# Kernel tuning notes

Measured on AMD Instinct MI355X. Metric: run time of the kernel, lower is better.

Reference implementation:

```python
import jax, jax.numpy as jnp
import numpy as np
from jax import lax

L, H = 16384, 1024
EPS = 1e-5


def _ln(x, w, b):
    m = jnp.mean(x, axis=-1, keepdims=True)
    v = jnp.var(x, axis=-1, keepdims=True)
    return (x - m) * lax.rsqrt(v + EPS) * w + b


def setup_inputs() -> dict:
    key = jax.random.key(0)
    ks = jax.random.split(key, 12)
    s = 0.02
    return {
        "x": jax.random.normal(ks[0], (L, H), dtype=jnp.float32),
        "ln1_w": jnp.ones((H,), jnp.float32),
        "ln1_b": jnp.zeros((H,), jnp.float32),
        "W_in": jax.random.normal(ks[1], (H, H), jnp.float32) * s,
        "b_in": jnp.zeros((H,), jnp.float32),
        "W_gate": jax.random.normal(ks[2], (H, H), jnp.float32) * s,
        "b_gate": jnp.zeros((H,), jnp.float32),
        "W_out": jax.random.normal(ks[3], (H, H), jnp.float32) * s,
        "b_out": jnp.zeros((H,), jnp.float32),
        "state_decay": jnp.zeros((H,), jnp.float32),
        "ln2_w": jnp.ones((H,), jnp.float32),
        "ln2_b": jnp.zeros((H,), jnp.float32),
        "W_ff1": jax.random.normal(ks[4], (H, 2 * H), jnp.float32) * s,
        "b_ff1": jnp.zeros((2 * H,), jnp.float32),
        "W_ff2": jax.random.normal(ks[5], (2 * H, H), jnp.float32) * s,
        "b_ff2": jnp.zeros((H,), jnp.float32),
    }


def reference(x, ln1_w, ln1_b, W_in, b_in, W_gate, b_gate, W_out, b_out,
              state_decay, ln2_w, ln2_b, W_ff1, b_ff1, W_ff2, b_ff2):
    hidden = _ln(x, ln1_w, ln1_b)                       # [L,H]
    u = hidden @ W_in + b_in                            # [L,H]
    gate = jax.nn.sigmoid(hidden @ W_gate + b_gate)     # [L,H]
    decay = jax.nn.sigmoid(state_decay)                 # [H]

    def step(s, u_t):
        s = decay * s + u_t
        return s, s

    z = jnp.zeros((x.shape[1],), x.dtype)
    _, states_f = lax.scan(step, z, u)                  # forward recurrence
    _, states_b = lax.scan(step, z, u, reverse=True)    # backward recurrence
    state_out = 0.5 * (states_f + states_b) * gate

    x = x + state_out @ W_out + b_out
    h = _ln(x, ln2_w, ln2_b)
    x = x + jax.nn.silu(h @ W_ff1 + b_ff1) @ W_ff2 + b_ff2
    return x
```

## Files before the change

kernel.cpp:

```cpp
#include <hip/hip_runtime.h>
#include <hip/hip_bf16.h>
#include <hip/hip_fp16.h>

#define L_SEQ 16384
#define HDIM  1024
#define CH    32
#define NC    (L_SEQ / CH)

typedef _Float16 f16;
typedef _Float16 f16x8 __attribute__((ext_vector_type(8)));
typedef _Float16 f16x4 __attribute__((ext_vector_type(4)));
typedef float    f32x4 __attribute__((ext_vector_type(4)));

#define AS1(p) (const __attribute__((address_space(1))) void*)(p)
#define AS3(p) (__attribute__((address_space(3))) void*)(p)

__global__ __launch_bounds__(256) void wcvt_t(const float* __restrict__ in,
                                              f16* __restrict__ out, int K, int N) {
  __shared__ float tile[32][33];
  int n0 = blockIdx.x * 32, k0 = blockIdx.y * 32;
  int tx = threadIdx.x, ty = threadIdx.y;
#pragma unroll
  for (int i = 0; i < 4; i++) {
    int k = k0 + ty + i * 8;
    tile[ty + i * 8][tx] = in[(size_t)k * N + n0 + tx];
  }
  __syncthreads();
#pragma unroll
  for (int i = 0; i < 4; i++) {
    int n = n0 + ty + i * 8;
    out[(size_t)n * K + k0 + tx] = (f16)tile[tx][ty + i * 8];
  }
}

__global__ __launch_bounds__(256) void ln_k(const float* __restrict__ x,
                                            const float* __restrict__ w,
                                            const float* __restrict__ b,
                                            f16* __restrict__ out,
                                            f16* __restrict__ xcopy) {
  int row = blockIdx.x;
  int t = threadIdx.x;
  const float4* xr = (const float4*)(x + (size_t)row * HDIM);
  float4 v = xr[t];
  float s  = v.x + v.y + v.z + v.w;
  float s2 = v.x * v.x + v.y * v.y + v.z * v.z + v.w * v.w;
#pragma unroll
  for (int off = 32; off > 0; off >>= 1) {
    s  += __shfl_down(s, off);
    s2 += __shfl_down(s2, off);
  }
  __shared__ float red[8];
  int wid = t >> 6, lane = t & 63;
  if (lane == 0) { red[wid] = s; red[4 + wid] = s2; }
  __syncthreads();
  if (t == 0) {
    red[0] = red[0] + red[1] + red[2] + red[3];
    red[4] = red[4] + red[5] + red[6] + red[7];
  }
  __syncthreads();
  float mean = red[0] * (1.0f / HDIM);
  float var  = red[4] * (1.0f / HDIM) - mean * mean;
  float rstd = rsqrtf(var + 1e-5f);
  float4 ww = ((const float4*)w)[t];
  float4 bb = ((const float4*)b)[t];
  f16x4 o;
  o[0] = (f16)((v.x - mean) * rstd * ww.x + bb.x);
  o[1] = (f16)((v.y - mean) * rstd * ww.y + bb.y);
  o[2] = (f16)((v.z - mean) * rstd * ww.z + bb.z);
  o[3] = (f16)((v.w - mean) * rstd * ww.w + bb.w);
  ((f16x4*)(out + (size_t)row * HDIM))[t] = o;
  if (xcopy) {
    f16x4 c;
    c[0] = (f16)v.x; c[1] = (f16)v.y; c[2] = (f16)v.z; c[3] = (f16)v.w;
    ((f16x4*)(xcopy + (size_t)row * HDIM))[t] = c;
  }
}

__global__ __launch_bounds__(128) void ln_k16(const f16* __restrict__ x,
                                              const float* __restrict__ w,
                                              const float* __restrict__ b,
                                              f16* __restrict__ out) {
  int row = blockIdx.x;
  int t = threadIdx.x;
  f16x8 xv = ((const f16x8*)(x + (size_t)row * HDIM))[t];
  float v[8];
  float s = 0.f, s2 = 0.f;
#pragma unroll
  for (int i = 0; i < 8; i++) {
    v[i] = (float)xv[i];
    s += v[i]; s2 += v[i] * v[i];
  }
#pragma unroll
  for (int off = 32; off > 0; off >>= 1) {
    s  += __shfl_down(s, off);
    s2 += __shfl_down(s2, off);
  }
  __shared__ float red[4];
  int wid = t >> 6, lane = t & 63;
  if (lane == 0) { red[wid] = s; red[2 + wid] = s2; }
  __syncthreads();
  float mean = (red[0] + red[1]) * (1.0f / HDIM);
  float var  = (red[2] + red[3]) * (1.0f / HDIM) - mean * mean;
  float rstd = rsqrtf(var + 1e-5f);
  float4 w1 = ((const float4*)w)[2 * t], w2 = ((const float4*)w)[2 * t + 1];
  float4 b1 = ((const float4*)b)[2 * t], b2 = ((const float4*)b)[2 * t + 1];
  float wv[8] = {w1.x, w1.y, w1.z, w1.w, w2.x, w2.y, w2.z, w2.w};
  float bv[8] = {b1.x, b1.y, b1.z, b1.w, b2.x, b2.y, b2.z, b2.w};
  f16x8 o;
#pragma unroll
  for (int i = 0; i < 8; i++) o[i] = (f16)((v[i] - mean) * rstd * wv[i] + bv[i]);
  ((f16x8*)(out + (size_t)row * HDIM))[t] = o;
}

template <int MODE, int RESID, int OUTF16>
__global__ __launch_bounds__(256, 4) void gemm_bt(const f16* __restrict__ A,
                                                  const f16* __restrict__ BT,
                                                  const float* __restrict__ bias,
                                                  const float* __restrict__ bias2,
                                                  const f16* __restrict__ resid,
                                                  void* __restrict__ Cout,
                                                  void* __restrict__ Cout2,
                                                  int M, int N, int K) {
  __shared__ __align__(16) f16 As[128 * 32];
  __shared__ __align__(16) f16 Bs[128 * 32];
  const int tid  = threadIdx.x;
  const int lane = tid & 63, wid = tid >> 6;
  const int wm = wid >> 1, wn = wid & 1;
  const int quad = lane >> 4, l16 = lane & 15;

  const int nbx = N >> 7, nby = M >> 7;
  const int b = blockIdx.x;
  const int xcd = b & 7;
  const int i = b >> 3;
  const int strips = nby >> 3;
  const int rs = i / nbx, cb = i - rs * nbx;
  const long m0 = (long)(xcd * strips + rs) << 7;
  const long n0 = (long)cb << 7;

  f32x4 zero = {0.f, 0.f, 0.f, 0.f};
  f32x4 acc[4][4];
#pragma unroll
  for (int i2 = 0; i2 < 4; i2++)
#pragma unroll
    for (int j = 0; j < 4; j++) acc[i2][j] = zero;

  for (int k0 = 0; k0 < K; k0 += 32) {
#pragma unroll
    for (int it = 0; it < 2; ++it) {
      int wboff = it * 4096 + wid * 1024;
      int eoff  = (wboff + lane * 16) >> 1;
      int r = eoff >> 5;
      int chunk = lane & 3;
      int src_c = ((chunk ^ (r & 3)) << 3);
      const f16* gA = A  + (m0 + r) * K + k0 + src_c;
      const f16* gB = BT + (n0 + r) * K + k0 + src_c;
      __builtin_amdgcn_global_load_lds(AS1(gA), AS3((char*)As + wboff), 16, 0, 0);
      __builtin_amdgcn_global_load_lds(AS1(gB), AS3((char*)Bs + wboff), 16, 0, 0);
    }
    __syncthreads();
    f16x8 af[4], bfr[4];
#pragma unroll
    for (int mi = 0; mi < 4; ++mi) {
      int row = wm * 64 + mi * 16 + l16;
      af[mi] = *(const f16x8*)(As + row * 32 + ((quad ^ (row & 3)) << 3));
    }
#pragma unroll
    for (int ni = 0; ni < 4; ++ni) {
      int row = wn * 64 + ni * 16 + l16;
      bfr[ni] = *(const f16x8*)(Bs + row * 32 + ((quad ^ (row & 3)) << 3));
    }
#pragma unroll
    for (int mi = 0; mi < 4; ++mi)
#pragma unroll
      for (int ni = 0; ni < 4; ++ni)
        acc[mi][ni] = __builtin_amdgcn_mfma_f32_16x16x32_f16(af[mi], bfr[ni], acc[mi][ni], 0, 0, 0);
    __syncthreads();
  }
#pragma unroll
  for (int mi = 0; mi < 4; ++mi) {
#pragma unroll
    for (int ni = 0; ni < 4; ++ni) {
      const long col = n0 + wn * 64 + ni * 16 + l16;
      float bc;
      if (MODE == 3) bc = (col < HDIM) ? bias[col] : bias2[col - HDIM];
      else           bc = bias[col];
#pragma unroll
      for (int r = 0; r < 4; ++r) {
        const long row = m0 + wm * 64 + mi * 16 + quad * 4 + r;
        float v = acc[mi][ni][r] + bc;
        if (MODE == 2) v = v / (1.f + __expf(-v));
        if (MODE == 3) {
          if (col < HDIM) {
            ((f16*)Cout)[row * HDIM + col] = (f16)v;
          } else {
            float g = 1.f / (1.f + __expf(-v));
            ((f16*)Cout2)[row * HDIM + (col - HDIM)] = (f16)g;
          }
        } else {
          if (RESID) v += (float)resid[row * N + col];
          if (OUTF16) ((f16*)Cout)[row * N + col] = (f16)v;
          else        ((float*)Cout)[row * N + col] = v;
        }
      }
    }
  }
}

__global__ __launch_bounds__(256) void scan_p1(const f16* __restrict__ u,
                                               const float* __restrict__ sdecay,
                                               float* __restrict__ carry_f,
                                               float* __restrict__ carry_b) {
  int tid = blockIdx.x * 256 + threadIdx.x;
  int h = tid & (HDIM - 1);
  int c = tid >> 10;
  float d = 1.f / (1.f + expf(-sdecay[h]));
  const f16* up = u + (size_t)c * CH * HDIM + h;
  float sf = 0.f, sb = 0.f, p = 1.f;
#pragma unroll
  for (int i = 0; i < CH; i++) {
    float uu = (float)up[i * HDIM];
    sf = d * sf + uu;
    sb += p * uu;
    p *= d;
  }
  carry_f[(size_t)c * HDIM + h] = sf;
  carry_b[(size_t)c * HDIM + h] = sb;
}

__global__ __launch_bounds__(256) void scan_p2(const float* __restrict__ sdecay,
                                               const float* __restrict__ carry_f,
                                               const float* __restrict__ carry_b,
                                               float* __restrict__ cin_f,
                                               float* __restrict__ cin_b) {
  int tid = blockIdx.x * 256 + threadIdx.x;
  int h = tid & (HDIM - 1);
  int dir = tid >> 10;
  float d = 1.f / (1.f + expf(-sdecay[h]));
  float dT = powf(d, (float)CH);
  float S = 0.f;
  if (dir == 0) {
#pragma unroll 4
    for (int c = 0; c < NC; c++) {
      cin_f[(size_t)c * HDIM + h] = S;
      S = dT * S + carry_f[(size_t)c * HDIM + h];
    }
  } else {
#pragma unroll 4
    for (int c = NC - 1; c >= 0; c--) {
      cin_b[(size_t)c * HDIM + h] = S;
      S = dT * S + carry_b[(size_t)c * HDIM + h];
    }
  }
}

__global__ __launch_bounds__(256) void scan_p3(const f16* __restrict__ u,
                                               const f16* __restrict__ gate,
                                               const float* __restrict__ sdecay,
                                               const float* __restrict__ cin_f,
                                               const float* __restrict__ cin_b,
                                               f16* __restrict__ state_out) {
  int tid = blockIdx.x * 256 + threadIdx.x;
  int h = tid & (HDIM - 1);
  int c = tid >> 10;
  float d = 1.f / (1.f + expf(-sdecay[h]));
  const f16* up = u    + (size_t)c * CH * HDIM + h;
  const f16* gp = gate + (size_t)c * CH * HDIM + h;
  f16* op = state_out  + (size_t)c * CH * HDIM + h;
  float ur[CH], sf[CH];
#pragma unroll
  for (int i = 0; i < CH; i++) ur[i] = (float)up[i * HDIM];
  float s = cin_f[(size_t)c * HDIM + h];
#pragma unroll
  for (int i = 0; i < CH; i++) { s = d * s + ur[i]; sf[i] = s; }
  s = cin_b[(size_t)c * HDIM + h];
#pragma unroll
  for (int i = CH - 1; i >= 0; i--) {
    s = d * s + ur[i];
    float g = (float)gp[i * HDIM];
    op[i * HDIM] = (f16)(0.5f * (sf[i] + s) * g);
  }
}

extern "C" void kernel_launch(void* const* d_in, const int* in_sizes, int n_in,
                              void* d_out, int out_size, void* d_ws, size_t ws_size,
                              hipStream_t stream) {
  const float* x      = (const float*)d_in[0];
  const float* ln1_w  = (const float*)d_in[1];
  const float* ln1_b  = (const float*)d_in[2];
  const float* W_in   = (const float*)d_in[3];
  const float* b_in   = (const float*)d_in[4];
  const float* W_gate = (const float*)d_in[5];
  const float* b_gate = (const float*)d_in[6];
  const float* W_out  = (const float*)d_in[7];
  const float* b_out  = (const float*)d_in[8];
  const float* sdecay = (const float*)d_in[9];
  const float* ln2_w  = (const float*)d_in[10];
  const float* ln2_b  = (const float*)d_in[11];
  const float* W_ff1  = (const float*)d_in[12];
  const float* b_ff1  = (const float*)d_in[13];
  const float* W_ff2  = (const float*)d_in[14];
  const float* b_ff2  = (const float*)d_in[15];
  float* out = (float*)d_out;

  char* ws = (char*)d_ws;
  const size_t MB32 = 33554432, MB64 = 67108864;
  f16* hidden = (f16*)(ws);
  f16* xh     = (f16*)(ws + MB32);
  f16* u      = (f16*)(ws + 2 * MB32);
  f16* gate   = (f16*)(ws + 3 * MB32);
  f16* x2h    = (f16*)(ws + 4 * MB32);
  f16* ff     = (f16*)(ws + 5 * MB32);
  char* wbase = ws + 5 * MB32 + MB64;
  f16* wt_ug  = (f16*)(wbase);
  f16* wt_out = (f16*)(wbase + 4194304);
  f16* wt_ff1 = (f16*)(wbase + 4194304 + 2097152);
  f16* wt_ff2 = (f16*)(wbase + 2 * 4194304 + 2097152);
  char* cbase = wbase + 3 * 4194304 + 2097152;
  float* carry_f = (float*)(cbase);
  float* carry_b = (float*)(cbase + 2097152);
  float* cin_f   = (float*)(cbase + 2 * 2097152);
  float* cin_b   = (float*)(cbase + 3 * 2097152);
  f16* state_out = hidden;
  f16* h2        = u;

  dim3 tb(32, 8);
  wcvt_t<<<dim3(32, 32), tb, 0, stream>>>(W_in,   wt_ug,                 1024, 1024);
  wcvt_t<<<dim3(32, 32), tb, 0, stream>>>(W_gate, wt_ug + 1024 * 1024,   1024, 1024);
  wcvt_t<<<dim3(32, 32), tb, 0, stream>>>(W_out,  wt_out,                1024, 1024);
  wcvt_t<<<dim3(64, 32), tb, 0, stream>>>(W_ff1,  wt_ff1,                1024, 2048);
  wcvt_t<<<dim3(32, 64), tb, 0, stream>>>(W_ff2,  wt_ff2,                2048, 1024);

  ln_k<<<L_SEQ, 256, 0, stream>>>(x, ln1_w, ln1_b, hidden, xh);

  gemm_bt<3, 0, 1><<<2048, 256, 0, stream>>>(hidden, wt_ug, b_in, b_gate, nullptr,
                                             u, gate, L_SEQ, 2048, 1024);

  scan_p1<<<2048, 256, 0, stream>>>(u, sdecay, carry_f, carry_b);
  scan_p2<<<8, 256, 0, stream>>>(sdecay, carry_f, carry_b, cin_f, cin_b);
  scan_p3<<<2048, 256, 0, stream>>>(u, gate, sdecay, cin_f, cin_b, state_out);

  gemm_bt<0, 1, 1><<<1024, 256, 0, stream>>>(state_out, wt_out, b_out, nullptr, xh,
                                             x2h, nullptr, L_SEQ, 1024, 1024);

  ln_k16<<<L_SEQ, 128, 0, stream>>>(x2h, ln2_w, ln2_b, h2);

  gemm_bt<2, 0, 1><<<2048, 256, 0, stream>>>(h2, wt_ff1, b_ff1, nullptr, nullptr,
                                             ff, nullptr, L_SEQ, 2048, 1024);

  gemm_bt<0, 1, 0><<<1024, 256, 0, stream>>>(ff, wt_ff2, b_ff2, nullptr, x2h,
                                             out, nullptr, L_SEQ, 1024, 2048);
}
```

Baseline: 599.0 us.

## Enlarge GEMM tiles to 256x256 with double-buffered LDS prefetch

The GEMM tile grows from 128x128 to 256x256 per block, giving each wave a 128x128 sub-tile of 64 accumulators. The K-loop now double-buffers the A and B tiles in LDS, prefetching the next K slice while the current one is computed, and drops one barrier per iteration. The XOR swizzle on LDS reads is removed, and occupancy drops to one block per CU (launch_bounds 256,1), with grids shrunk accordingly. The aim is more data reuse per load and latency hiding, at the risk of heavy register pressure (256 accumulator floats per thread), LDS bank conflicts without the swizzle, and fewer blocks (256 to 512) across the CUs.

```diff
diff --git a/kernel.cpp b/kernel.cpp
--- a/kernel.cpp
+++ b/kernel.cpp
@@ -113,7 +113,7 @@
 }
 
 template <int MODE, int RESID, int OUTF16>
-__global__ __launch_bounds__(256, 4) void gemm_bt(const f16* __restrict__ A,
+__global__ __launch_bounds__(256, 1) void gemm_bt(const f16* __restrict__ A,
                                                   const f16* __restrict__ BT,
                                                   const float* __restrict__ bias,
                                                   const float* __restrict__ bias2,
@@ -121,72 +121,82 @@
                                                   void* __restrict__ Cout,
                                                   void* __restrict__ Cout2,
                                                   int M, int N, int K) {
-  __shared__ __align__(16) f16 As[128 * 32];
-  __shared__ __align__(16) f16 Bs[128 * 32];
+  __shared__ __align__(16) f16 As[2][256 * 32];
+  __shared__ __align__(16) f16 Bs[2][256 * 32];
   const int tid  = threadIdx.x;
   const int lane = tid & 63, wid = tid >> 6;
   const int wm = wid >> 1, wn = wid & 1;
   const int quad = lane >> 4, l16 = lane & 15;
 
-  const int nbx = N >> 7, nby = M >> 7;
+  const int nbx = N >> 8, nby = M >> 8;
   const int b = blockIdx.x;
   const int xcd = b & 7;
   const int i = b >> 3;
   const int strips = nby >> 3;
   const int rs = i / nbx, cb = i - rs * nbx;
-  const long m0 = (long)(xcd * strips + rs) << 7;
-  const long n0 = (long)cb << 7;
+  const long m0 = (long)(xcd * strips + rs) << 8;
+  const long n0 = (long)cb << 8;
+
+  const int srow = wid * 16 + (lane >> 2);
+  const int scol = (lane & 3) * 8;
+  const f16* gA = A  + (m0 + srow) * K + scol;
+  const f16* gB = BT + (n0 + srow) * K + scol;
+  const int sdst = wid * 1024;
 
   f32x4 zero = {0.f, 0.f, 0.f, 0.f};
-  f32x4 acc[4][4];
-#pragma unroll
-  for (int i2 = 0; i2 < 4; i2++)
-#pragma unroll
-    for (int j = 0; j < 4; j++) acc[i2][j] = zero;
+  f32x4 acc[8][8];
+#pragma unroll
+  for (int i2 = 0; i2 < 8; i2++)
+#pragma unroll
+    for (int j = 0; j < 8; j++) acc[i2][j] = zero;
+
+#pragma unroll
+  for (int it = 0; it < 4; ++it) {
+    __builtin_amdgcn_global_load_lds(AS1(gA + (size_t)(it * 64) * K),
+                                     AS3((char*)As[0] + it * 4096 + sdst), 16, 0, 0);
+    __builtin_amdgcn_global_load_lds(AS1(gB + (size_t)(it * 64) * K),
+                                     AS3((char*)Bs[0] + it * 4096 + sdst), 16, 0, 0);
+  }
+  __syncthreads();
 
   for (int k0 = 0; k0 < K; k0 += 32) {
-#pragma unroll
-    for (int it = 0; it < 2; ++it) {
-      int wboff = it * 4096 + wid * 1024;
-      int eoff  = (wboff + lane * 16) >> 1;
-      int r = eoff >> 5;
-      int chunk = lane & 3;
-      int src_c = ((chunk ^ (r & 3)) << 3);
-      const f16* gA = A  + (m0 + r) * K + k0 + src_c;
-      const f16* gB = BT + (n0 + r) * K + k0 + src_c;
-      __builtin_amdgcn_global_load_lds(AS1(gA), AS3((char*)As + wboff), 16, 0, 0);
-      __builtin_amdgcn_global_load_lds(AS1(gB), AS3((char*)Bs + wboff), 16, 0, 0);
+    const int cur = (k0 >> 5) & 1;
+    if (k0 + 32 < K) {
+      const int nxt = cur ^ 1;
+#pragma unroll
+      for (int it = 0; it < 4; ++it) {
+        __builtin_amdgcn_global_load_lds(AS1(gA + (size_t)(it * 64) * K + (k0 + 32)),
+                                         AS3((char*)As[nxt] + it * 4096 + sdst), 16, 0, 0);
+        __builtin_amdgcn_global_load_lds(AS1(gB + (size_t)(it * 64) * K + (k0 + 32)),
+                                         AS3((char*)Bs[nxt] + it * 4096 + sdst), 16, 0, 0);
+      }
     }
-    __syncthreads();
-    f16x8 af[4], bfr[4];
-#pragma unroll
-    for (int mi = 0; mi < 4; ++mi) {
-      int row = wm * 64 + mi * 16 + l16;
-      af[mi] = *(const f16x8*)(As + row * 32 + ((quad ^ (row & 3)) << 3));
-    }
-#pragma unroll
-    for (int ni = 0; ni < 4; ++ni) {
-      int row = wn * 64 + ni * 16 + l16;
-      bfr[ni] = *(const f16x8*)(Bs + row * 32 + ((quad ^ (row & 3)) << 3));
-    }
-#pragma unroll
-    for (int mi = 0; mi < 4; ++mi)
-#pragma unroll
-      for (int ni = 0; ni < 4; ++ni)
+    f16x8 af[8], bfr[8];
+#pragma unroll
+    for (int mi = 0; mi < 8; ++mi)
+      af[mi] = *(const f16x8*)(As[cur] + (wm * 128 + mi * 16 + l16) * 32 + quad * 8);
+#pragma unroll
+    for (int ni = 0; ni < 8; ++ni)
+      bfr[ni] = *(const f16x8*)(Bs[cur] + (wn * 128 + ni * 16 + l16) * 32 + quad * 8);
+#pragma unroll
+    for (int mi = 0; mi < 8; ++mi)
+#pragma unroll
+      for (int ni = 0; ni < 8; ++ni)
         acc[mi][ni] = __builtin_amdgcn_mfma_f32_16x16x32_f16(af[mi], bfr[ni], acc[mi][ni], 0, 0, 0);
     __syncthreads();
   }
-#pragma unroll
-  for (int mi = 0; mi < 4; ++mi) {
-#pragma unroll
-    for (int ni = 0; ni < 4; ++ni) {
-      const long col = n0 + wn * 64 + ni * 16 + l16;
+
+#pragma unroll
+  for (int mi = 0; mi < 8; ++mi) {
+#pragma unroll
+    for (int ni = 0; ni < 8; ++ni) {
+      const long col = n0 + wn * 128 + ni * 16 + l16;
       float bc;
       if (MODE == 3) bc = (col < HDIM) ? bias[col] : bias2[col - HDIM];
       else           bc = bias[col];
 #pragma unroll
       for (int r = 0; r < 4; ++r) {
-        const long row = m0 + wm * 64 + mi * 16 + quad * 4 + r;
+        const long row = m0 + wm * 128 + mi * 16 + quad * 4 + r;
         float v = acc[mi][ni][r] + bc;
         if (MODE == 2) v = v / (1.f + __expf(-v));
         if (MODE == 3) {
@@ -332,21 +342,21 @@
 
   ln_k<<<L_SEQ, 256, 0, stream>>>(x, ln1_w, ln1_b, hidden, xh);
 
-  gemm_bt<3, 0, 1><<<2048, 256, 0, stream>>>(hidden, wt_ug, b_in, b_gate, nullptr,
-                                             u, gate, L_SEQ, 2048, 1024);
+  gemm_bt<3, 0, 1><<<512, 256, 0, stream>>>(hidden, wt_ug, b_in, b_gate, nullptr,
+                                            u, gate, L_SEQ, 2048, 1024);
 
   scan_p1<<<2048, 256, 0, stream>>>(u, sdecay, carry_f, carry_b);
   scan_p2<<<8, 256, 0, stream>>>(sdecay, carry_f, carry_b, cin_f, cin_b);
   scan_p3<<<2048, 256, 0, stream>>>(u, gate, sdecay, cin_f, cin_b, state_out);
 
-  gemm_bt<0, 1, 1><<<1024, 256, 0, stream>>>(state_out, wt_out, b_out, nullptr, xh,
-                                             x2h, nullptr, L_SEQ, 1024, 1024);
+  gemm_bt<0, 1, 1><<<256, 256, 0, stream>>>(state_out, wt_out, b_out, nullptr, xh,
+                                            x2h, nullptr, L_SEQ, 1024, 1024);
 
   ln_k16<<<L_SEQ, 128, 0, stream>>>(x2h, ln2_w, ln2_b, h2);
 
-  gemm_bt<2, 0, 1><<<2048, 256, 0, stream>>>(h2, wt_ff1, b_ff1, nullptr, nullptr,
-                                             ff, nullptr, L_SEQ, 2048, 1024);
-
-  gemm_bt<0, 1, 0><<<1024, 256, 0, stream>>>(ff, wt_ff2, b_ff2, nullptr, x2h,
-                                             out, nullptr, L_SEQ, 1024, 2048);
-}
+  gemm_bt<2, 0, 1><<<512, 256, 0, stream>>>(h2, wt_ff1, b_ff1, nullptr, nullptr,
+                                            ff, nullptr, L_SEQ, 2048, 1024);
+
+  gemm_bt<0, 1, 0><<<256, 256, 0, stream>>>(ff, wt_ff2, b_ff2, nullptr, x2h,
+                                            out, nullptr, L_SEQ, 1024, 2048);
+}
```

Measured after the change: 797.1 us. 33.1% more time.

## Double-buffer GEMM LDS tiles and drop XOR swizzle

Applied to the files above, without the earlier changes.

The GEMM now keeps two LDS buffers for the A and B tiles and issues the async global-to-LDS loads for the next K step before computing on the current one. This overlaps memory latency with MFMA work and needs only one barrier per iteration. The XOR bank swizzle is removed in favour of a plain row layout with precomputed pointers, which may bring back LDS bank conflicts. Doubling LDS to 32KB per block may also lower occupancy.

```diff
diff --git a/kernel.cpp b/kernel.cpp
--- a/kernel.cpp
+++ b/kernel.cpp
@@ -121,8 +121,8 @@
                                                   void* __restrict__ Cout,
                                                   void* __restrict__ Cout2,
                                                   int M, int N, int K) {
-  __shared__ __align__(16) f16 As[128 * 32];
-  __shared__ __align__(16) f16 Bs[128 * 32];
+  __shared__ __align__(16) f16 As[2][128 * 32];
+  __shared__ __align__(16) f16 Bs[2][128 * 32];
   const int tid  = threadIdx.x;
   const int lane = tid & 63, wid = tid >> 6;
   const int wm = wid >> 1, wn = wid & 1;
@@ -137,6 +137,12 @@
   const long m0 = (long)(xcd * strips + rs) << 7;
   const long n0 = (long)cb << 7;
 
+  const int srow = wid * 16 + (lane >> 2);
+  const int scol = (lane & 3) * 8;
+  const f16* gA = A  + (m0 + srow) * K + scol;
+  const f16* gB = BT + (n0 + srow) * K + scol;
+  const int sdst = wid * 1024;
+
   f32x4 zero = {0.f, 0.f, 0.f, 0.f};
   f32x4 acc[4][4];
 #pragma unroll
@@ -144,31 +150,36 @@
 #pragma unroll
     for (int j = 0; j < 4; j++) acc[i2][j] = zero;
 
-  for (int k0 = 0; k0 < K; k0 += 32) {
-#pragma unroll
-    for (int it = 0; it < 2; ++it) {
-      int wboff = it * 4096 + wid * 1024;
-      int eoff  = (wboff + lane * 16) >> 1;
-      int r = eoff >> 5;
-      int chunk = lane & 3;
-      int src_c = ((chunk ^ (r & 3)) << 3);
-      const f16* gA = A  + (m0 + r) * K + k0 + src_c;
-      const f16* gB = BT + (n0 + r) * K + k0 + src_c;
-      __builtin_amdgcn_global_load_lds(AS1(gA), AS3((char*)As + wboff), 16, 0, 0);
-      __builtin_amdgcn_global_load_lds(AS1(gB), AS3((char*)Bs + wboff), 16, 0, 0);
+#pragma unroll
+  for (int it = 0; it < 2; ++it) {
+    __builtin_amdgcn_global_load_lds(AS1(gA + (size_t)(it * 64) * K),
+                                     AS3((char*)As[0] + it * 4096 + sdst), 16, 0, 0);
+    __builtin_amdgcn_global_load_lds(AS1(gB + (size_t)(it * 64) * K),
+                                     AS3((char*)Bs[0] + it * 4096 + sdst), 16, 0, 0);
+  }
+  __syncthreads();
+
+  const int niter = K >> 5;
+  for (int ki = 0; ki < niter; ++ki) {
+    const int cur = ki & 1;
+    if (ki + 1 < niter) {
+      const int nxt = cur ^ 1;
+      const int koff = (ki + 1) << 5;
+#pragma unroll
+      for (int it = 0; it < 2; ++it) {
+        __builtin_amdgcn_global_load_lds(AS1(gA + (size_t)(it * 64) * K + koff),
+                                         AS3((char*)As[nxt] + it * 4096 + sdst), 16, 0, 0);
+        __builtin_amdgcn_global_load_lds(AS1(gB + (size_t)(it * 64) * K + koff),
+                                         AS3((char*)Bs[nxt] + it * 4096 + sdst), 16, 0, 0);
+      }
     }
-    __syncthreads();
     f16x8 af[4], bfr[4];
 #pragma unroll
-    for (int mi = 0; mi < 4; ++mi) {
-      int row = wm * 64 + mi * 16 + l16;
-      af[mi] = *(const f16x8*)(As + row * 32 + ((quad ^ (row & 3)) << 3));
-    }
-#pragma unroll
-    for (int ni = 0; ni < 4; ++ni) {
-      int row = wn * 64 + ni * 16 + l16;
-      bfr[ni] = *(const f16x8*)(Bs + row * 32 + ((quad ^ (row & 3)) << 3));
-    }
+    for (int mi = 0; mi < 4; ++mi)
+      af[mi] = *(const f16x8*)(As[cur] + (wm * 64 + mi * 16 + l16) * 32 + quad * 8);
+#pragma unroll
+    for (int ni = 0; ni < 4; ++ni)
+      bfr[ni] = *(const f16x8*)(Bs[cur] + (wn * 64 + ni * 16 + l16) * 32 + quad * 8);
 #pragma unroll
     for (int mi = 0; mi < 4; ++mi)
 #pragma unroll
@@ -176,6 +187,7 @@
         acc[mi][ni] = __builtin_amdgcn_mfma_f32_16x16x32_f16(af[mi], bfr[ni], acc[mi][ni], 0, 0, 0);
     __syncthreads();
   }
+
 #pragma unroll
   for (int mi = 0; mi < 4; ++mi) {
 #pragma unroll
```

New measurement: 595.6 us. Within noise of the previous version (-0.6%).
